# Kernel optimization log

Hardware: AMD Instinct MI355X
Metric: run time of the kernel (lower is better)

Reference implementation:

```python
import jax, jax.numpy as jnp
import numpy as np

EMBED = 100
BATCH = 4096
NUM_NEG = 256
U, P, W, RP, B, C = 30000, 50000, 100000, 50000, 5000, 1000


def _tab(k, v, e=EMBED):
    r = 0.5 / e
    w = jax.random.uniform(k, (v + 1, e), minval=-r, maxval=r, dtype=jnp.float32)
    return w.at[-1].set(0.0)  # padding row is zeros, as in torch code


def setup_inputs() -> dict:
    key = jax.random.key(0)
    ks = jax.random.split(key, 10)
    inp = {
        'user_emb': _tab(ks[0], U),
        'product_emb': _tab(ks[1], P),
        'word_emb': _tab(ks[2], W),
        'brand_emb': _tab(ks[3], B),
        'category_emb': _tab(ks[4], C),
        'rproduct_emb': _tab(ks[5], RP),
        'rel_vecs': jax.random.uniform(ks[6], (8, EMBED), minval=-0.5 / EMBED, maxval=0.5 / EMBED, dtype=jnp.float32),
        'purchase_bias': jnp.zeros((P + 1,), jnp.float32),
        'mentions_bias': jnp.zeros((W + 1,), jnp.float32),
        'describe_bias': jnp.zeros((W + 1,), jnp.float32),
        'produced_bias': jnp.zeros((B + 1,), jnp.float32),
        'belongs_bias': jnp.zeros((C + 1,), jnp.float32),
        'also_bought_bias': jnp.zeros((RP + 1,), jnp.float32),
        'also_viewed_bias': jnp.zeros((RP + 1,), jnp.float32),
        'together_bias': jnp.zeros((RP + 1,), jnp.float32),
    }
    # batch_idxs columns: (u, p, w, b, c, rp1, rp2, rp3), each in its own vocab range
    col_max = [U, P, W, B, C, RP, RP, RP]
    cols = [jax.random.randint(jax.random.fold_in(ks[7], i), (BATCH,), 0, m) for i, m in enumerate(col_max)]
    inp['batch_idxs'] = jnp.stack(cols, axis=1)
    # deterministic stand-in for torch.multinomial negative sampling, one row per relation
    neg_max = [P, W, W, B, C, RP, RP, RP]
    negs = [jax.random.randint(jax.random.fold_in(ks[8], i), (NUM_NEG,), 0, m) for i, m in enumerate(neg_max)]
    inp['neg_idxs'] = jnp.stack(negs, axis=0)
    return inp


def _neg_loss(head_tab, tail_tab, rvec, bias_tab, h, t, n):
    hv = head_tab[h]                      # [B,E] gather
    ex = hv + rvec                        # [B,E]
    tv = tail_tab[t]                      # [B,E]
    bias = bias_tab[t]                    # [B]
    pos = jnp.sum(ex * tv, axis=-1) + bias  # bmm([B,1,E],[B,E,1]) == rowwise dot
    nv = tail_tab[n]                      # [N,E]
    neg = jnp.einsum('be,ne->bn', ex, nv) + bias[:, None]  # [B,N]
    pos_loss = -jax.nn.log_sigmoid(pos)   # == -log(sigmoid(pos)), stable
    neg_loss = -jax.nn.log_sigmoid(-neg).sum(axis=1)
    return (pos_loss + neg_loss).mean()


def reference(batch_idxs, neg_idxs, user_emb, product_emb, word_emb, brand_emb,
              category_emb, rproduct_emb, rel_vecs, purchase_bias, mentions_bias,
              describe_bias, produced_bias, belongs_bias, also_bought_bias,
              also_viewed_bias, together_bias):
    # (head_tab, tail_tab, bias_tab, head_col, tail_col) per relation, in original order
    rels = [
        (user_emb, product_emb, purchase_bias, 0, 1),
        (user_emb, word_emb, mentions_bias, 0, 2),
        (product_emb, word_emb, describe_bias, 1, 2),
        (product_emb, brand_emb, produced_bias, 1, 3),
        (product_emb, category_emb, belongs_bias, 1, 4),
        (product_emb, rproduct_emb, also_bought_bias, 1, 5),
        (product_emb, rproduct_emb, also_viewed_bias, 1, 6),
        (product_emb, rproduct_emb, together_bias, 1, 7),
    ]
    loss = jnp.float32(0.0)
    for r, (ht, tt, bt, hc, tc) in enumerate(rels):
        loss = loss + _neg_loss(ht, tt, rel_vecs[r], bt,
                                batch_idxs[:, hc], batch_idxs[:, tc], neg_idxs[r])
    return loss
```

## Files before the change

### kernel.cpp

```cpp
#include <hip/hip_runtime.h>


#define EMBED   100
#define BATCH   4096
#define NUM_NEG 256
#define BM      64
#define BN      128
#define PITCH   136

typedef __attribute__((ext_vector_type(8))) short s8;
typedef __attribute__((ext_vector_type(4))) short s4;
typedef __attribute__((ext_vector_type(4))) float f4;

struct RelP {
    const float* head;
    const float* tail;
    const float* bias;
    int hc, tc;
};

struct Params {
    RelP rel[8];
    const float* rel_vecs;
    const int*   batch_idxs;
    const int*   neg_idxs;
    float*       out;
};

__device__ __forceinline__ float softplus_f(float x) {
    float e = __expf(-fabsf(x));
    return fmaxf(x, 0.0f) + __logf(1.0f + e);
}

__device__ __forceinline__ unsigned short bf16_rne(float f) {
    unsigned u = __float_as_uint(f);
    u += 0x7FFFu + ((u >> 16) & 1u);
    return (unsigned short)(u >> 16);
}

__device__ __forceinline__ float bf16_to_f(short s) {
    return __uint_as_float(((unsigned)(unsigned short)s) << 16);
}

__launch_bounds__(256, 3)
__global__ void ke_kernel(Params p) {
    const int bid = blockIdx.x;
    const int r   = bid & 7;
    const int rb  = (bid >> 3) & 63;
    const int nb  = bid >> 9;
    const int tid = threadIdx.x;

    __shared__ __align__(16) short As[BM * PITCH];
    __shared__ __align__(16) short Bs[BN * PITCH];

    const RelP rp = p.rel[r];

    if (tid < 192) {
        const bool isA = tid < BM;
        const float* src;
        unsigned short extra;
        short* dst;
        if (isA) {
            const int grow = rb * BM + tid;
            const int h  = p.batch_idxs[grow * 8 + rp.hc];
            const int ti = p.batch_idxs[grow * 8 + rp.tc];
            src   = rp.head + (size_t)h * EMBED;
            extra = bf16_rne(rp.bias[ti]);
            dst   = As + tid * PITCH;
        } else {
            const int n = p.neg_idxs[r * NUM_NEG + nb * BN + (tid - BM)];
            src   = rp.tail + (size_t)n * EMBED;
            extra = 0x3F80;
            dst   = Bs + (tid - BM) * PITCH;
        }
        const float4* s4p = (const float4*)src;
        const float4* rv4 = (const float4*)(p.rel_vecs + r * EMBED);

#pragma unroll
        for (int j = 0; j < 12; ++j) {
            float4 f0 = s4p[2 * j];
            float4 f1 = s4p[2 * j + 1];
            if (isA) {
                const float4 a = rv4[2 * j];
                const float4 b = rv4[2 * j + 1];
                f0.x += a.x; f0.y += a.y; f0.z += a.z; f0.w += a.w;
                f1.x += b.x; f1.y += b.y; f1.z += b.z; f1.w += b.w;
            }
            s8 v = { (short)bf16_rne(f0.x), (short)bf16_rne(f0.y),
                     (short)bf16_rne(f0.z), (short)bf16_rne(f0.w),
                     (short)bf16_rne(f1.x), (short)bf16_rne(f1.y),
                     (short)bf16_rne(f1.z), (short)bf16_rne(f1.w) };
            *(s8*)(dst + 8 * j) = v;
        }
        {
            float4 f = s4p[24];
            if (isA) {
                const float4 a = rv4[24];
                f.x += a.x; f.y += a.y; f.z += a.z; f.w += a.w;
            }
            s4 v = { (short)bf16_rne(f.x), (short)bf16_rne(f.y),
                     (short)bf16_rne(f.z), (short)bf16_rne(f.w) };
            *(s4*)(dst + 96) = v;
        }
        {
            s4 v = { (short)extra, 0, 0, 0 };
            *(s4*)(dst + 100) = v;
            s4 z = { 0, 0, 0, 0 };
#pragma unroll
            for (int j = 0; j < 6; ++j)
                *(s4*)(dst + 104 + 4 * j) = z;
        }
    }

    const bool doPos = (nb == 0) && (tid >= 192);
    const int  prow  = rb * BM + (tid - 192);
    const float* ptail = rp.tail;
    float pbias = 0.0f;
    if (doPos) {
        const int pt = p.batch_idxs[prow * 8 + rp.tc];
        ptail = rp.tail + (size_t)pt * EMBED;
        pbias = rp.bias[pt];
    }

    __syncthreads();

    const int wave = tid >> 6;
    const int lane = tid & 63;
    const int li   = lane & 15;
    const int q    = lane >> 4;
    const int wm   = wave & 1;
    const int wn   = wave >> 1;

    f4 acc[2][4];
#pragma unroll
    for (int i = 0; i < 2; ++i)
#pragma unroll
        for (int j = 0; j < 4; ++j)
            acc[i][j] = (f4){0.f, 0.f, 0.f, 0.f};

    const short* Abase = As + (wm * 32 + li) * PITCH + q * 8;
    const short* Bbase = Bs + (wn * 64 + li) * PITCH + q * 8;

#pragma unroll
    for (int s = 0; s < 4; ++s) {
        const s8 a0 = *(const s8*)(Abase +  0 * PITCH + s * 32);
        const s8 a1 = *(const s8*)(Abase + 16 * PITCH + s * 32);
        const s8 b0 = *(const s8*)(Bbase +  0 * PITCH + s * 32);
        const s8 b1 = *(const s8*)(Bbase + 16 * PITCH + s * 32);
        const s8 b2 = *(const s8*)(Bbase + 32 * PITCH + s * 32);
        const s8 b3 = *(const s8*)(Bbase + 48 * PITCH + s * 32);
        acc[0][0] = __builtin_amdgcn_mfma_f32_16x16x32_bf16(a0, b0, acc[0][0], 0, 0, 0);
        acc[0][1] = __builtin_amdgcn_mfma_f32_16x16x32_bf16(a0, b1, acc[0][1], 0, 0, 0);
        acc[0][2] = __builtin_amdgcn_mfma_f32_16x16x32_bf16(a0, b2, acc[0][2], 0, 0, 0);
        acc[0][3] = __builtin_amdgcn_mfma_f32_16x16x32_bf16(a0, b3, acc[0][3], 0, 0, 0);
        acc[1][0] = __builtin_amdgcn_mfma_f32_16x16x32_bf16(a1, b0, acc[1][0], 0, 0, 0);
        acc[1][1] = __builtin_amdgcn_mfma_f32_16x16x32_bf16(a1, b1, acc[1][1], 0, 0, 0);
        acc[1][2] = __builtin_amdgcn_mfma_f32_16x16x32_bf16(a1, b2, acc[1][2], 0, 0, 0);
        acc[1][3] = __builtin_amdgcn_mfma_f32_16x16x32_bf16(a1, b3, acc[1][3], 0, 0, 0);
    }

    float local = 0.0f;
#pragma unroll
    for (int i = 0; i < 2; ++i)
#pragma unroll
        for (int j = 0; j < 4; ++j) {
            local += softplus_f(acc[i][j].x);
            local += softplus_f(acc[i][j].y);
            local += softplus_f(acc[i][j].z);
            local += softplus_f(acc[i][j].w);
        }

    if (doPos) {
        const short* exr = As + (tid - 192) * PITCH;
        const float4* tv = (const float4*)ptail;
        float d0 = 0.f, d1 = 0.f, d2 = 0.f, d3 = 0.f;
#pragma unroll
        for (int j = 0; j < 25; ++j) {
            const s4 e = *(const s4*)(exr + 4 * j);
            const float4 v = tv[j];
            d0 = fmaf(bf16_to_f(e.x), v.x, d0);
            d1 = fmaf(bf16_to_f(e.y), v.y, d1);
            d2 = fmaf(bf16_to_f(e.z), v.z, d2);
            d3 = fmaf(bf16_to_f(e.w), v.w, d3);
        }
        const float pos = ((d0 + d1) + (d2 + d3)) + pbias;
        local += softplus_f(-pos);
    }

#pragma unroll
    for (int off = 32; off > 0; off >>= 1)
        local += __shfl_down(local, off, 64);

    __syncthreads();
    float* wsum = (float*)Bs;
    if (lane == 0) wsum[wave] = local;
    __syncthreads();
    if (tid == 0) {
        const float s = (wsum[0] + wsum[1]) + (wsum[2] + wsum[3]);
        atomicAdd(p.out, s * (1.0f / BATCH));
    }
}

extern "C" void kernel_launch(void* const* d_in, const int* in_sizes, int n_in,
                              void* d_out, int out_size, void* d_ws, size_t ws_size,
                              hipStream_t stream) {
    const float* user  = (const float*)d_in[0];
    const float* prod  = (const float*)d_in[1];
    const float* word  = (const float*)d_in[2];
    const float* brand = (const float*)d_in[3];
    const float* cat   = (const float*)d_in[4];
    const float* rprod = (const float*)d_in[5];

    Params p;
    p.rel_vecs   = (const float*)d_in[6];
    p.batch_idxs = (const int*)d_in[15];
    p.neg_idxs   = (const int*)d_in[16];
    p.out        = (float*)d_out;

    p.rel[0] = {user, prod,  (const float*)d_in[7],  0, 1};
    p.rel[1] = {user, word,  (const float*)d_in[8],  0, 2};
    p.rel[2] = {prod, word,  (const float*)d_in[9],  1, 2};
    p.rel[3] = {prod, brand, (const float*)d_in[10], 1, 3};
    p.rel[4] = {prod, cat,   (const float*)d_in[11], 1, 4};
    p.rel[5] = {prod, rprod, (const float*)d_in[12], 1, 5};
    p.rel[6] = {prod, rprod, (const float*)d_in[13], 1, 6};
    p.rel[7] = {prod, rprod, (const float*)d_in[14], 1, 7};

    hipMemsetAsync(d_out, 0, sizeof(float), stream);
    ke_kernel<<<1024, 256, 0, stream>>>(p);
}
```

Baseline: 162.4 us.

## Split gather/convert into prep kernel writing bf16 tiles to workspace

```diff
diff --git a/kernel.cpp b/kernel.cpp
--- a/kernel.cpp
+++ b/kernel.cpp
@@ -42,8 +42,72 @@
     return __uint_as_float(((unsigned)(unsigned short)s) << 16);
 }
 
+__launch_bounds__(256, 4)
+__global__ void ke_prep(Params p, short* aws, short* bws) {
+    const int id  = blockIdx.x * 256 + threadIdx.x;
+    const bool isA = id < 32768;
+    const int r = isA ? (id >> 12) : ((id - 32768) >> 8);
+    const RelP rp = p.rel[r];
+
+    const float* src;
+    unsigned short extra;
+    short* dst;
+    if (isA) {
+        const int row = id & 4095;
+        const int h  = p.batch_idxs[row * 8 + rp.hc];
+        const int ti = p.batch_idxs[row * 8 + rp.tc];
+        src   = rp.head + (size_t)h * EMBED;
+        extra = bf16_rne(rp.bias[ti]);
+        dst   = aws + (size_t)id * PITCH;
+    } else {
+        const int j = id - 32768;
+        const int n = p.neg_idxs[(j >> 8) * NUM_NEG + (j & 255)];
+        src   = rp.tail + (size_t)n * EMBED;
+        extra = 0x3F80;
+        dst   = bws + (size_t)j * PITCH;
+    }
+
+    const float4* s4p = (const float4*)src;
+    const float4* rv4 = (const float4*)(p.rel_vecs + r * EMBED);
+
+#pragma unroll
+    for (int j = 0; j < 12; ++j) {
+        float4 f0 = s4p[2 * j];
+        float4 f1 = s4p[2 * j + 1];
+        if (isA) {
+            const float4 a = rv4[2 * j];
+            const float4 b = rv4[2 * j + 1];
+            f0.x += a.x; f0.y += a.y; f0.z += a.z; f0.w += a.w;
+            f1.x += b.x; f1.y += b.y; f1.z += b.z; f1.w += b.w;
+        }
+        s8 v = { (short)bf16_rne(f0.x), (short)bf16_rne(f0.y),
+                 (short)bf16_rne(f0.z), (short)bf16_rne(f0.w),
+                 (short)bf16_rne(f1.x), (short)bf16_rne(f1.y),
+                 (short)bf16_rne(f1.z), (short)bf16_rne(f1.w) };
+        *(s8*)(dst + 8 * j) = v;
+    }
+    {
+        float4 f = s4p[24];
+        if (isA) {
+            const float4 a = rv4[24];
+            f.x += a.x; f.y += a.y; f.z += a.z; f.w += a.w;
+        }
+        s4 v = { (short)bf16_rne(f.x), (short)bf16_rne(f.y),
+                 (short)bf16_rne(f.z), (short)bf16_rne(f.w) };
+        *(s4*)(dst + 96) = v;
+    }
+    {
+        s4 v = { (short)extra, 0, 0, 0 };
+        *(s4*)(dst + 100) = v;
+        s8 z = { 0,0,0,0,0,0,0,0 };
+#pragma unroll
+        for (int j = 0; j < 4; ++j)
+            *(s8*)(dst + 104 + 8 * j) = z;
+    }
+}
+
 __launch_bounds__(256, 3)
-__global__ void ke_kernel(Params p) {
+__global__ void ke_main(Params p, const short* aws, const short* bws) {
     const int bid = blockIdx.x;
     const int r   = bid & 7;
     const int rb  = (bid >> 3) & 63;
@@ -55,68 +119,27 @@
 
     const RelP rp = p.rel[r];
 
-    if (tid < 192) {
-        const bool isA = tid < BM;
-        const float* src;
-        unsigned short extra;
-        short* dst;
-        if (isA) {
-            const int grow = rb * BM + tid;
-            const int h  = p.batch_idxs[grow * 8 + rp.hc];
-            const int ti = p.batch_idxs[grow * 8 + rp.tc];
-            src   = rp.head + (size_t)h * EMBED;
-            extra = bf16_rne(rp.bias[ti]);
-            dst   = As + tid * PITCH;
-        } else {
-            const int n = p.neg_idxs[r * NUM_NEG + nb * BN + (tid - BM)];
-            src   = rp.tail + (size_t)n * EMBED;
-            extra = 0x3F80;
-            dst   = Bs + (tid - BM) * PITCH;
-        }
-        const float4* s4p = (const float4*)src;
-        const float4* rv4 = (const float4*)(p.rel_vecs + r * EMBED);
-
-#pragma unroll
-        for (int j = 0; j < 12; ++j) {
-            float4 f0 = s4p[2 * j];
-            float4 f1 = s4p[2 * j + 1];
-            if (isA) {
-                const float4 a = rv4[2 * j];
-                const float4 b = rv4[2 * j + 1];
-                f0.x += a.x; f0.y += a.y; f0.z += a.z; f0.w += a.w;
-                f1.x += b.x; f1.y += b.y; f1.z += b.z; f1.w += b.w;
-            }
-            s8 v = { (short)bf16_rne(f0.x), (short)bf16_rne(f0.y),
-                     (short)bf16_rne(f0.z), (short)bf16_rne(f0.w),
-                     (short)bf16_rne(f1.x), (short)bf16_rne(f1.y),
-                     (short)bf16_rne(f1.z), (short)bf16_rne(f1.w) };
-            *(s8*)(dst + 8 * j) = v;
-        }
-        {
-            float4 f = s4p[24];
-            if (isA) {
-                const float4 a = rv4[24];
-                f.x += a.x; f.y += a.y; f.z += a.z; f.w += a.w;
-            }
-            s4 v = { (short)bf16_rne(f.x), (short)bf16_rne(f.y),
-                     (short)bf16_rne(f.z), (short)bf16_rne(f.w) };
-            *(s4*)(dst + 96) = v;
-        }
-        {
-            s4 v = { (short)extra, 0, 0, 0 };
-            *(s4*)(dst + 100) = v;
-            s4 z = { 0, 0, 0, 0 };
-#pragma unroll
-            for (int j = 0; j < 6; ++j)
-                *(s4*)(dst + 104 + 4 * j) = z;
-        }
+    {
+        const s8* asrc = (const s8*)(aws + (size_t)(r * 4096 + rb * BM) * PITCH);
+        s8* adst = (s8*)As;
+#pragma unroll
+        for (int j = 0; j < 4; ++j)
+            adst[tid + 256 * j] = asrc[tid + 256 * j];
+        if (tid < 64) adst[1024 + tid] = asrc[1024 + tid];
+
+        const s8* bsrc = (const s8*)(bws + (size_t)(r * NUM_NEG + nb * BN) * PITCH);
+        s8* bdst = (s8*)Bs;
+#pragma unroll
+        for (int j = 0; j < 8; ++j)
+            bdst[tid + 256 * j] = bsrc[tid + 256 * j];
+        if (tid < 128) bdst[2048 + tid] = bsrc[2048 + tid];
     }
 
     const bool doPos = (nb == 0) && (tid >= 192);
-    const int  prow  = rb * BM + (tid - 192);
     const float* ptail = rp.tail;
     float pbias = 0.0f;
     if (doPos) {
+        const int prow = rb * BM + (tid - 192);
         const int pt = p.batch_idxs[prow * 8 + rp.tc];
         ptail = rp.tail + (size_t)pt * EMBED;
         pbias = rp.bias[pt];
@@ -226,6 +249,10 @@
     p.rel[6] = {prod, rprod, (const float*)d_in[13], 1, 6};
     p.rel[7] = {prod, rprod, (const float*)d_in[14], 1, 7};
 
+    short* aws = (short*)d_ws;
+    short* bws = aws + (size_t)32768 * PITCH;
+
     hipMemsetAsync(d_out, 0, sizeof(float), stream);
-    ke_kernel<<<1024, 256, 0, stream>>>(p);
-}
+    ke_prep<<<136, 256, 0, stream>>>(p, aws, bws);
+    ke_main<<<1024, 256, 0, stream>>>(p, aws, bws);
+}
```

Result: slower. 169.0 us (+4.1%).
